# Optimization experiments

Measured on AMD Instinct MI355X. Metric: run time of the kernel, lower is better.

The kernel has to match this reference:

```python
import jax, jax.numpy as jnp
import numpy as np

B, S, D, H = 2, 2048, 1024, 16
HD = D // H  # 64
MASK_VAL = -10000.0


def setup_inputs() -> dict:
    key = jax.random.key(0)
    ks = jax.random.split(key, 8)
    sc = 0.02
    q_features = jax.random.normal(ks[0], (B, S, D), jnp.float32)
    kv_features = jax.random.normal(ks[1], (B, S, D), jnp.float32)
    # causal mask, broadcastable (1,1,S,S)
    mask = jnp.tril(jnp.ones((S, S), jnp.bool_))[None, None]
    Wq = jax.random.normal(ks[2], (D, D), jnp.float32) * sc
    bq = jnp.zeros((D,), jnp.float32)
    Wkv = jax.random.normal(ks[3], (D, 2 * D), jnp.float32) * sc
    bkv = jnp.zeros((2 * D,), jnp.float32)
    Wp = jax.random.normal(ks[4], (D, D), jnp.float32) * sc
    bp = jnp.zeros((D,), jnp.float32)
    return {"q_features": q_features, "kv_features": kv_features, "mask": mask,
            "Wq": Wq, "bq": bq, "Wkv": Wkv, "bkv": bkv, "Wp": Wp, "bp": bp}


def _split_heads(t):
    # (B,S,D) -> (B,H,S,HD)
    return t.reshape(B, S, H, HD).transpose(0, 2, 1, 3)


def reference(q_features, kv_features, mask, Wq, bq, Wkv, bkv, Wp, bp):
    query = q_features @ Wq + bq            # (B,S,D)
    kv = kv_features @ Wkv + bkv            # (B,S,2D)
    key, value = jnp.split(kv, 2, axis=-1)
    q = _split_heads(query)                 # (B,H,S,HD)
    k = _split_heads(key)
    v = _split_heads(value)
    scores = jnp.einsum('bhqd,bhkd->bhqk', q, k) / jnp.sqrt(jnp.float32(HD))
    scores = jnp.where(mask, scores, jnp.asarray(MASK_VAL, scores.dtype))
    attn = jax.nn.softmax(scores, axis=-1)  # (B,H,S,S)
    out = jnp.einsum('bhqk,bhkd->bhqd', attn, v)
    out = out.transpose(0, 2, 1, 3).reshape(B, S, D)  # merge heads
    return out @ Wp + bp
```

## Files before the change

### kernel.cpp

```cpp
#include <hip/hip_runtime.h>

typedef unsigned short u16;
typedef unsigned int u32;
typedef __attribute__((ext_vector_type(4))) unsigned short us4;
typedef __attribute__((ext_vector_type(8))) unsigned short us8;
typedef __attribute__((ext_vector_type(4))) short s16x4;
typedef __attribute__((ext_vector_type(8))) __bf16 bf16x8;
typedef __attribute__((ext_vector_type(4))) float floatx4;

#define S_ 2048
#define D_ 1024
#define QSC 0.18033688f

__device__ __forceinline__ float b2f(u16 u) {
  unsigned v = ((unsigned)u) << 16;
  return __builtin_bit_cast(float, v);
}
__device__ __forceinline__ u16 f2bf(float f) {
  unsigned u = __builtin_bit_cast(unsigned, f);
  unsigned r = (u + 0x7fffu + ((u >> 16) & 1u)) >> 16;
  return (u16)r;
}
__device__ __forceinline__ u16 f2bf_rhu(float f) {
  return (u16)((__builtin_bit_cast(unsigned, f) + 0x8000u) >> 16);
}

typedef const __attribute__((address_space(1))) u32* gas_t;
typedef __attribute__((address_space(3))) u32* las_t;
__device__ __forceinline__ void gload16(const u16* g, u16* l) {
  __builtin_amdgcn_global_load_lds((gas_t)g, (las_t)l, 16, 0, 0);
}

__global__ __launch_bounds__(256) void prep(
    const float* __restrict__ qf, const float* __restrict__ kvf,
    const float* __restrict__ Wq, const float* __restrict__ Wkv,
    const float* __restrict__ Wp, u16* __restrict__ qa, u16* __restrict__ kva,
    u16* __restrict__ Wqt, u16* __restrict__ Wkvt, u16* __restrict__ Wpt) {
  int bid = blockIdx.x, tid = threadIdx.x;
  if (bid < 4096) {
    const float* src = (bid < 2048) ? qf : kvf;
    u16* dst = (bid < 2048) ? qa : kva;
    size_t i = ((size_t)(bid & 2047) * 256 + tid) * 8;
    floatx4 a = *(const floatx4*)(src + i);
    floatx4 b = *(const floatx4*)(src + i + 4);
    us8 r;
#pragma unroll
    for (int j = 0; j < 4; j++) { r[j] = f2bf(a[j]); r[4 + j] = f2bf(b[j]); }
    *(us8*)(dst + i) = r;
  } else {
    int t = bid - 4096;
    const float* src; u16* dst; int R, C;
    if (t < 1024)      { src = Wq;  dst = Wqt;  R = 1024; C = 1024; }
    else if (t < 3072) { t -= 1024; src = Wkv; dst = Wkvt; R = 1024; C = 2048; }
    else               { t -= 3072; src = Wp;  dst = Wpt;  R = 1024; C = 1024; }
    int bx = t % (C >> 5), by = t / (C >> 5);
    __shared__ u16 tile[32][33];
    int tx = tid & 31, ty = tid >> 5;
    int x = bx * 32 + tx;
    for (int i = ty; i < 32; i += 8)
      tile[i][tx] = f2bf(src[(size_t)(by * 32 + i) * C + x]);
    __syncthreads();
    int ox = by * 32 + tx;
    for (int i = ty; i < 32; i += 8)
      dst[(size_t)(bx * 32 + i) * R + ox] = tile[tx][i];
  }
}

template <int TM, int TN, int MODE>
__device__ __forceinline__ void gemm_core(
    const u16* __restrict__ A, const u16* __restrict__ Bt,
    const float* __restrict__ bias, void* __restrict__ C0,
    u16* __restrict__ C1, int N, int n0, int m0,
    u16* As, u16* Bs, float cscale) {
  constexpr int MT = TM / 32, NT = TN / 32;
  int tid  = threadIdx.x;
  int wave = tid >> 6, lane = tid & 63;
  int quad = lane >> 4, l16 = lane & 15;
  int wr = wave >> 1, wc = wave & 1;
  const u16* Ag = A  + (size_t)(m0 + wave * 8 + (lane >> 3)) * 1024 + (lane & 7) * 8;
  const u16* Bg = Bt + (size_t)(n0 + wave * 8 + (lane >> 3)) * 1024 + (lane & 7) * 8;
  u16* Aw = As + wave * 8 * 64;
  u16* Bw = Bs + wave * 8 * 64;
  floatx4 acc[MT][NT] = {};
  for (int k0 = 0; k0 < 1024; k0 += 64) {
    if (k0) __syncthreads();
#pragma unroll
    for (int p = 0; p < TM / 32; p++)
      gload16(Ag + (size_t)p * 32 * 1024 + k0, Aw + p * 32 * 64);
#pragma unroll
    for (int p = 0; p < TN / 32; p++)
      gload16(Bg + (size_t)p * 32 * 1024 + k0, Bw + p * 32 * 64);
    __syncthreads();
#pragma unroll
    for (int kk = 0; kk < 2; kk++) {
      bf16x8 af[MT], bf[NT];
#pragma unroll
      for (int mt = 0; mt < MT; mt++)
        af[mt] = __builtin_bit_cast(bf16x8,
            *(const us8*)&As[(wr * (TM / 2) + mt * 16 + l16) * 64 + (kk * 4 + quad) * 8]);
#pragma unroll
      for (int nt = 0; nt < NT; nt++)
        bf[nt] = __builtin_bit_cast(bf16x8,
            *(const us8*)&Bs[(wc * (TN / 2) + nt * 16 + l16) * 64 + (kk * 4 + quad) * 8]);
#pragma unroll
      for (int mt = 0; mt < MT; mt++)
#pragma unroll
        for (int nt = 0; nt < NT; nt++)
          acc[mt][nt] = __builtin_amdgcn_mfma_f32_16x16x32_bf16(
              af[mt], bf[nt], acc[mt][nt], 0, 0, 0);
    }
  }
#pragma unroll
  for (int mt = 0; mt < MT; mt++) {
#pragma unroll
    for (int nt = 0; nt < NT; nt++) {
      int col  = n0 + wc * (TN / 2) + nt * 16 + l16;
      int rowq = m0 + wr * (TM / 2) + mt * 16 + quad * 4;
      float bv = bias[col];
      if (MODE == 0) {
        u16* o = (u16*)C0;
#pragma unroll
        for (int r = 0; r < 4; r++)
          o[(size_t)(rowq + r) * N + col] = f2bf((acc[mt][nt][r] + bv) * cscale);
      } else if (MODE == 1) {
        float* o = (float*)C0;
#pragma unroll
        for (int r = 0; r < 4; r++)
          o[(size_t)(rowq + r) * N + col] = acc[mt][nt][r] + bv;
      } else {
        if (col < 1024) {
          u16* o = (u16*)C0;
#pragma unroll
          for (int r = 0; r < 4; r++)
            o[(size_t)(rowq + r) * 1024 + col] = f2bf(acc[mt][nt][r] + bv);
        } else {
          int vcol = col - 1024;
          int b = rowq >> 11, s0 = rowq & 2047;
          us4 pv;
#pragma unroll
          for (int r = 0; r < 4; r++) pv[r] = f2bf(acc[mt][nt][r] + bv);
          *(us4*)&C1[((size_t)(b * 1024 + vcol)) * (size_t)S_ + s0] = pv;
        }
      }
    }
  }
}

__global__ __launch_bounds__(256) void gemm_qkv(
    const u16* __restrict__ qa, const u16* __restrict__ kva,
    const u16* __restrict__ Wqt, const u16* __restrict__ Wkvt,
    const float* __restrict__ bq, const float* __restrict__ bkv,
    u16* __restrict__ Qb, u16* __restrict__ Kb, u16* __restrict__ Vt) {
  __shared__ __align__(16) u16 As[128 * 64];
  __shared__ __align__(16) u16 Bs[128 * 64];
  int bid = blockIdx.x;
  if (bid < 256) {
    gemm_core<128, 128, 0>(qa, Wqt, bq, Qb, nullptr, 1024,
                           (bid & 7) * 128, (bid >> 3) * 128, As, Bs, QSC);
  } else {
    int lb = bid - 256;
    gemm_core<128, 128, 2>(kva, Wkvt, bkv, Kb, Vt, 2048,
                           (lb & 15) * 128, (lb >> 4) * 128, As, Bs, 1.0f);
  }
}

__global__ __launch_bounds__(256) void gemm_out(
    const u16* __restrict__ AO, const u16* __restrict__ Wpt,
    const float* __restrict__ bp, float* __restrict__ out) {
  __shared__ __align__(16) u16 As[64 * 64];
  __shared__ __align__(16) u16 Bs[128 * 64];
  gemm_core<64, 128, 1>(AO, Wpt, bp, out, nullptr, 1024,
                        (blockIdx.x & 7) * 128, (blockIdx.x >> 3) * 64, As, Bs, 1.0f);
}

__global__ __launch_bounds__(256) void attn_fwd(
    const u16* __restrict__ Q, const u16* __restrict__ Kb,
    const u16* __restrict__ Vt, u16* __restrict__ O,
    u16* __restrict__ Opart, float* __restrict__ ml) {
  __shared__ __align__(16) u16 Ks[64 * 64];
  __shared__ __align__(16) u16 Vs[64 * 64];
  int tid  = threadIdx.x;
  int wave = tid >> 6, lane = tid & 63;
  int quad = lane >> 4, l16 = lane & 15;
  int bh = blockIdx.x, b = bh >> 4, h = bh & 15;
  int y = blockIdx.y;
  int qt, kb0, kb1, half = 0;
  bool split = (y < 32);
  if (split) {
    qt = 31 - (y >> 1);
    half = y & 1;
    int h1 = (qt + 1) >> 1;
    kb0 = half ? h1 : 0;
    kb1 = half ? (qt + 1) : h1;
  } else {
    qt = 47 - y;
    kb0 = 0; kb1 = qt + 1;
  }
  const size_t row0 = (size_t)b * S_;
  const u16* Kg = Kb + row0 * D_ + h * 64;
  const u16* Vg = Vt + ((size_t)b * 1024 + h * 64) * S_;

  int qrow = qt * 64 + wave * 16 + l16;
  const u16* qp = Q + (row0 + qrow) * D_ + h * 64 + quad * 8;
  bf16x8 aqv[2];
  aqv[0] = __builtin_bit_cast(bf16x8, *(const us8*)(qp));
  aqv[1] = __builtin_bit_cast(bf16x8, *(const us8*)(qp + 32));

  floatx4 o_[4] = {};
  floatx4 l_acc = {};
  const s16x4 ones4 = {0x3F80, 0x3F80, 0x3F80, 0x3F80};

  int lr = lane >> 3, c8 = lane & 7;
  int r0 = wave * 16 + lr;
  int r1 = r0 + 8;
  us8 pk0 = *(const us8*)(Kg + (size_t)(kb0 * 64 + r0) * D_ + c8 * 8);
  us8 pk1 = *(const us8*)(Kg + (size_t)(kb0 * 64 + r1) * D_ + c8 * 8);
  us8 pv0 = *(const us8*)(Vg + (size_t)r0 * S_ + kb0 * 64 + c8 * 8);
  us8 pv1 = *(const us8*)(Vg + (size_t)r1 * S_ + kb0 * 64 + c8 * 8);

  for (int kb = kb0; kb < kb1; kb++) {
    __syncthreads();
    *(us8*)&Ks[r0 * 64 + ((c8 ^ (r0 & 7)) << 3)] = pk0;
    *(us8*)&Ks[r1 * 64 + ((c8 ^ (r1 & 7)) << 3)] = pk1;
    *(us8*)&Vs[r0 * 64 + ((c8 ^ (r0 & 7)) << 3)] = pv0;
    *(us8*)&Vs[r1 * 64 + ((c8 ^ (r1 & 7)) << 3)] = pv1;
    if (kb + 1 < kb1) {
      int koff = (kb + 1) * 64;
      pk0 = *(const us8*)(Kg + (size_t)(koff + r0) * D_ + c8 * 8);
      pk1 = *(const us8*)(Kg + (size_t)(koff + r1) * D_ + c8 * 8);
      pv0 = *(const us8*)(Vg + (size_t)r0 * S_ + koff + c8 * 8);
      pv1 = *(const us8*)(Vg + (size_t)r1 * S_ + koff + c8 * 8);
    }
    __syncthreads();

    floatx4 s[4] = {};
#pragma unroll
    for (int kk = 0; kk < 2; kk++)
#pragma unroll
      for (int nt = 0; nt < 4; nt++) {
        us8 kf = *(const us8*)&Ks[(nt * 16 + l16) * 64 +
                                  (((kk * 4 + quad) ^ (l16 & 7)) << 3)];
        s[nt] = __builtin_amdgcn_mfma_f32_16x16x32_bf16(
            __builtin_bit_cast(bf16x8, kf), aqv[kk], s[nt], 0, 0, 0);
      }

    if (kb == qt) {
      int qg = wave * 16 + l16;
#pragma unroll
      for (int nt = 0; nt < 4; nt++)
#pragma unroll
        for (int r = 0; r < 4; r++)
          if (nt * 16 + quad * 4 + r > qg) s[nt][r] = -1e5f;
    }

    s16x4 pb[4];
#pragma unroll
    for (int nt = 0; nt < 4; nt++)
#pragma unroll
      for (int r = 0; r < 4; r++)
        pb[nt][r] = (short)f2bf_rhu(__builtin_amdgcn_exp2f(s[nt][r]));

#pragma unroll
    for (int nt = 0; nt < 4; nt++) {
      l_acc = __builtin_amdgcn_mfma_f32_16x16x16bf16_1k(ones4, pb[nt], l_acc, 0, 0, 0);
#pragma unroll
      for (int mt = 0; mt < 4; mt++) {
        int hd = mt * 16 + l16;
        int chunk = nt * 2 + (quad >> 1);
        us4 vf = *(const us4*)&Vs[hd * 64 + ((chunk ^ (l16 & 7)) << 3) + (quad & 1) * 4];
        o_[mt] = __builtin_amdgcn_mfma_f32_16x16x16bf16_1k(
            __builtin_bit_cast(s16x4, vf), pb[nt], o_[mt], 0, 0, 0);
      }
    }
  }

  if (!split) {
    float rl = __builtin_amdgcn_rcpf(l_acc[0]);
    size_t orow = (row0 + qt * 64 + wave * 16 + l16) * D_ + h * 64;
#pragma unroll
    for (int mt = 0; mt < 4; mt++) {
      us4 ov;
#pragma unroll
      for (int r = 0; r < 4; r++) ov[r] = f2bf(o_[mt][r] * rl);
      *(us4*)&O[orow + mt * 16 + quad * 4] = ov;
    }
  } else {
    int pb_ = (qt - 16) * 2 + half;
    u16* op = Opart + ((size_t)(bh * 32 + pb_)) * 4096;
    int qrow_l = wave * 16 + l16;
#pragma unroll
    for (int mt = 0; mt < 4; mt++) {
      us4 ov;
#pragma unroll
      for (int r = 0; r < 4; r++) ov[r] = f2bf(o_[mt][r]);
      *(us4*)&op[qrow_l * 64 + mt * 16 + quad * 4] = ov;
    }
    if (quad == 0)
      ml[(size_t)(bh * 32 + pb_) * 64 + qrow_l] = l_acc[0];
  }
}

__global__ __launch_bounds__(256) void combine(
    const u16* __restrict__ Opart, const float* __restrict__ ml,
    u16* __restrict__ O) {
  int bh = blockIdx.x, b = bh >> 4, h = bh & 15;
  int qt = 16 + blockIdx.y;
  int base = bh * 32 + (qt - 16) * 2;
  const u16* o1 = Opart + (size_t)base * 4096;
  const u16* o2 = o1 + 4096;
  int row = threadIdx.x >> 2, cg = (threadIdx.x & 3) * 16;
  float l1 = ml[(size_t)base * 64 + row];
  float l2 = ml[(size_t)(base + 1) * 64 + row];
  float inv = __builtin_amdgcn_rcpf(l1 + l2);
  size_t orow = ((size_t)b * S_ + qt * 64 + row) * D_ + h * 64 + cg;
#pragma unroll
  for (int v = 0; v < 2; v++) {
    us8 x1 = *(const us8*)&o1[row * 64 + cg + v * 8];
    us8 x2 = *(const us8*)&o2[row * 64 + cg + v * 8];
    us8 out;
#pragma unroll
    for (int j = 0; j < 8; j++)
      out[j] = f2bf((b2f(x1[j]) + b2f(x2[j])) * inv);
    *(us8*)&O[orow + v * 8] = out;
  }
}

extern "C" void kernel_launch(void* const* d_in, const int* in_sizes, int n_in,
                              void* d_out, int out_size, void* d_ws, size_t ws_size,
                              hipStream_t stream) {
  const float* qf  = (const float*)d_in[0];
  const float* kvf = (const float*)d_in[1];
  const float* Wq  = (const float*)d_in[3];
  const float* bq  = (const float*)d_in[4];
  const float* Wkv = (const float*)d_in[5];
  const float* bkv = (const float*)d_in[6];
  const float* Wp  = (const float*)d_in[7];
  const float* bp  = (const float*)d_in[8];

  char* ws = (char*)d_ws;
  const size_t MB = 1048576;
  u16*   kva  = (u16*)(ws);
  u16*   AO   = (u16*)(ws);
  u16*   Kbp  = (u16*)(ws + 8 * MB);
  u16*   Vtp  = (u16*)(ws + 16 * MB);
  u16*   Wqt  = (u16*)(ws + 24 * MB);
  float* mlp  = (float*)(ws + 24 * MB);
  u16*   Wkvt = (u16*)(ws + 26 * MB);
  u16*   Wpt  = (u16*)(ws + 30 * MB);
  u16*   qa    = (u16*)d_out;
  u16*   Opart = (u16*)d_out;
  u16*   Qb    = (u16*)d_out + (size_t)4 * 1048576;

  prep<<<8192, 256, 0, stream>>>(qf, kvf, Wq, Wkv, Wp, qa, kva, Wqt, Wkvt, Wpt);
  gemm_qkv<<<768, 256, 0, stream>>>(qa, kva, Wqt, Wkvt, bq, bkv, Qb, Kbp, Vtp);
  attn_fwd<<<dim3(32, 48), 256, 0, stream>>>(Qb, Kbp, Vtp, AO, Opart, mlp);
  combine<<<dim3(32, 16), 256, 0, stream>>>(Opart, mlp, AO);
  gemm_out<<<512, 256, 0, stream>>>(AO, Wpt, bp, (float*)d_out);
}
```

Baseline: 229.0 us.

## Rewrite QKV GEMM as 256x256 tile with 4-stage async LDS pipeline

Replaces the 128x128 QKV projection GEMM with a 512-thread kernel computing 256x256 tiles. It uses a 4-stage ring of direct global-to-LDS loads with XOR-swizzled layout, split A/B phases with barriers, and raised priority around MFMA bursts. The aim is to raise data reuse per tile and hide global-load latency behind MFMA work. The cost is a 128KB LDS footprint and only 192 blocks, which can leave CUs underused and weakens occupancy.

Result: faster. 217.4 us (-5.0%).

```diff
diff --git a/kernel.cpp b/kernel.cpp
--- a/kernel.cpp
+++ b/kernel.cpp
@@ -30,6 +30,16 @@
 __device__ __forceinline__ void gload16(const u16* g, u16* l) {
   __builtin_amdgcn_global_load_lds((gas_t)g, (las_t)l, 16, 0, 0);
 }
+
+#define PBAR()                                   \
+  {                                              \
+    __builtin_amdgcn_sched_barrier(0);           \
+    asm volatile("" ::: "memory");               \
+    __builtin_amdgcn_s_barrier();                \
+    asm volatile("" ::: "memory");               \
+    __builtin_amdgcn_sched_barrier(0);           \
+  }
+#define WAITVM(N) asm volatile("s_waitcnt vmcnt(" #N ")" ::: "memory")
 
 __global__ __launch_bounds__(256) void prep(
     const float* __restrict__ qf, const float* __restrict__ kvf,
@@ -66,6 +76,148 @@
   }
 }
 
+template <int MODE>
+__device__ __forceinline__ void gemm256(
+    const u16* __restrict__ A, const u16* __restrict__ Bt,
+    const float* __restrict__ bias, void* __restrict__ C0,
+    u16* __restrict__ C1, int N, int m0, int n0, u16* smem, float cscale) {
+  int tid = threadIdx.x;
+  int w = tid >> 6, lane = tid & 63;
+  int quad = lane >> 4, l16 = lane & 15;
+  int wr = w >> 2, wc = w & 3;
+
+  int srow = w * 32 + (lane >> 2);
+  int gchunk = ((lane & 3) ^ ((lane >> 3) & 3)) << 3;
+  const u16* Asrc = A + (size_t)(m0 + srow) * 1024 + gchunk;
+  const u16* Bsrc = Bt + (size_t)(n0 + srow) * 1024 + gchunk;
+  u16* Adst = smem + w * 1024;
+  u16* Bdst = smem + 32768 + w * 1024;
+
+  int swz = (quad ^ ((l16 >> 1) & 3)) << 3;
+  int aoff = (wr * 128 + l16) * 32 + swz;
+  int boff = 32768 + (wc * 64 + l16) * 32 + swz;
+
+  floatx4 acc[8][4] = {};
+
+#define STAGE_A(t)                                             \
+  {                                                            \
+    int s_ = (t) & 3;                                          \
+    gload16(Asrc + (t) * 32, Adst + s_ * 8192);                \
+    gload16(Asrc + (t) * 32 + 16384, Adst + s_ * 8192 + 512);  \
+  }
+#define STAGE_B(t)                                             \
+  {                                                            \
+    int s_ = (t) & 3;                                          \
+    gload16(Bsrc + (t) * 32, Bdst + s_ * 8192);                \
+    gload16(Bsrc + (t) * 32 + 16384, Bdst + s_ * 8192 + 512);  \
+  }
+
+  STAGE_A(0); STAGE_B(0); STAGE_A(1); STAGE_B(1); STAGE_A(2); STAGE_B(2);
+  WAITVM(8);
+  PBAR();
+
+  bf16x8 af[4], bf[4];
+
+#define PHASE_A(t, DOSTAGE)                                                 \
+  {                                                                         \
+    int s_ = (t) & 3;                                                       \
+    _Pragma("unroll") for (int mf = 0; mf < 4; mf++)                        \
+        af[mf] = __builtin_bit_cast(                                        \
+            bf16x8, *(const us8*)&smem[s_ * 8192 + aoff + mf * 512]);       \
+    _Pragma("unroll") for (int nf = 0; nf < 4; nf++)                        \
+        bf[nf] = __builtin_bit_cast(                                        \
+            bf16x8, *(const us8*)&smem[s_ * 8192 + boff + nf * 512]);       \
+    if (DOSTAGE) STAGE_A((t) + 3);                                          \
+    PBAR();                                                                 \
+    __builtin_amdgcn_s_setprio(1);                                          \
+    _Pragma("unroll") for (int mf = 0; mf < 4; mf++)                        \
+        _Pragma("unroll") for (int nf = 0; nf < 4; nf++)                    \
+            acc[mf][nf] = __builtin_amdgcn_mfma_f32_16x16x32_bf16(          \
+                af[mf], bf[nf], acc[mf][nf], 0, 0, 0);                      \
+    __builtin_amdgcn_s_setprio(0);                                          \
+    PBAR();                                                                 \
+  }
+#define PHASE_B(t, DOSTAGE, VMW)                                            \
+  {                                                                         \
+    int s_ = (t) & 3;                                                       \
+    _Pragma("unroll") for (int mf = 0; mf < 4; mf++)                        \
+        af[mf] = __builtin_bit_cast(                                        \
+            bf16x8,                                                         \
+            *(const us8*)&smem[s_ * 8192 + aoff + 2048 + mf * 512]);        \
+    if (DOSTAGE) STAGE_B((t) + 3);                                          \
+    PBAR();                                                                 \
+    __builtin_amdgcn_s_setprio(1);                                          \
+    _Pragma("unroll") for (int mf = 0; mf < 4; mf++)                        \
+        _Pragma("unroll") for (int nf = 0; nf < 4; nf++)                    \
+            acc[4 + mf][nf] = __builtin_amdgcn_mfma_f32_16x16x32_bf16(      \
+                af[mf], bf[nf], acc[4 + mf][nf], 0, 0, 0);                  \
+    __builtin_amdgcn_s_setprio(0);                                          \
+    VMW;                                                                    \
+    PBAR();                                                                 \
+  }
+
+#pragma unroll 1
+  for (int t = 0; t < 29; t++) {
+    PHASE_A(t, true);
+    PHASE_B(t, true, WAITVM(4));
+  }
+  PHASE_A(29, false); PHASE_B(29, false, (void)0);
+  PHASE_A(30, false); PHASE_B(30, false, WAITVM(0));
+  PHASE_A(31, false); PHASE_B(31, false, (void)0);
+
+#undef PHASE_A
+#undef PHASE_B
+#undef STAGE_A
+#undef STAGE_B
+
+#pragma unroll
+  for (int mf = 0; mf < 8; mf++) {
+#pragma unroll
+    for (int nf = 0; nf < 4; nf++) {
+      int col = n0 + wc * 64 + nf * 16 + l16;
+      int rowq = m0 + wr * 128 + mf * 16 + quad * 4;
+      float bv = bias[col];
+      if (MODE == 0) {
+        u16* o = (u16*)C0;
+#pragma unroll
+        for (int r = 0; r < 4; r++)
+          o[(size_t)(rowq + r) * N + col] = f2bf((acc[mf][nf][r] + bv) * cscale);
+      } else {
+        if (col < 1024) {
+          u16* o = (u16*)C0;
+#pragma unroll
+          for (int r = 0; r < 4; r++)
+            o[(size_t)(rowq + r) * 1024 + col] = f2bf(acc[mf][nf][r] + bv);
+        } else {
+          int vcol = col - 1024;
+          int b = rowq >> 11, s0 = rowq & 2047;
+          us4 pv;
+#pragma unroll
+          for (int r = 0; r < 4; r++) pv[r] = f2bf(acc[mf][nf][r] + bv);
+          *(us4*)&C1[((size_t)(b * 1024 + vcol)) * (size_t)S_ + s0] = pv;
+        }
+      }
+    }
+  }
+}
+
+__global__ __launch_bounds__(512, 2) void gemm_qkv(
+    const u16* __restrict__ qa, const u16* __restrict__ kva,
+    const u16* __restrict__ Wqt, const u16* __restrict__ Wkvt,
+    const float* __restrict__ bq, const float* __restrict__ bkv,
+    u16* __restrict__ Qb, u16* __restrict__ Kb, u16* __restrict__ Vt) {
+  __shared__ __align__(16) u16 smem[65536];
+  int bid = blockIdx.x;
+  if (bid < 64) {
+    gemm256<0>(qa, Wqt, bq, Qb, nullptr, 1024,
+               (bid >> 2) * 256, (bid & 3) * 256, smem, QSC);
+  } else {
+    int lb = bid - 64;
+    gemm256<2>(kva, Wkvt, bkv, Kb, Vt, 2048,
+               (lb >> 3) * 256, (lb & 7) * 256, smem, 1.0f);
+  }
+}
+
 template <int TM, int TN, int MODE>
 __device__ __forceinline__ void gemm_core(
     const u16* __restrict__ A, const u16* __restrict__ Bt,
@@ -143,24 +295,6 @@
         }
       }
     }
-  }
-}
-
-__global__ __launch_bounds__(256) void gemm_qkv(
-    const u16* __restrict__ qa, const u16* __restrict__ kva,
-    const u16* __restrict__ Wqt, const u16* __restrict__ Wkvt,
-    const float* __restrict__ bq, const float* __restrict__ bkv,
-    u16* __restrict__ Qb, u16* __restrict__ Kb, u16* __restrict__ Vt) {
-  __shared__ __align__(16) u16 As[128 * 64];
-  __shared__ __align__(16) u16 Bs[128 * 64];
-  int bid = blockIdx.x;
-  if (bid < 256) {
-    gemm_core<128, 128, 0>(qa, Wqt, bq, Qb, nullptr, 1024,
-                           (bid & 7) * 128, (bid >> 3) * 128, As, Bs, QSC);
-  } else {
-    int lb = bid - 256;
-    gemm_core<128, 128, 2>(kva, Wkvt, bkv, Kb, Vt, 2048,
-                           (lb & 15) * 128, (lb >> 4) * 128, As, Bs, 1.0f);
   }
 }
 
@@ -352,7 +486,7 @@
   u16*   Qb    = (u16*)d_out + (size_t)4 * 1048576;
 
   prep<<<8192, 256, 0, stream>>>(qf, kvf, Wq, Wkv, Wp, qa, kva, Wqt, Wkvt, Wpt);
-  gemm_qkv<<<768, 256, 0, stream>>>(qa, kva, Wqt, Wkvt, bq, bkv, Qb, Kbp, Vtp);
+  gemm_qkv<<<192, 512, 0, stream>>>(qa, kva, Wqt, Wkvt, bq, bkv, Qb, Kbp, Vtp);
   attn_fwd<<<dim3(32, 48), 256, 0, stream>>>(Qb, Kbp, Vtp, AO, Opart, mlp);
   combine<<<dim3(32, 16), 256, 0, stream>>>(Opart, mlp, AO);
   gemm_out<<<512, 256, 0, stream>>>(AO, Wpt, bp, (float*)d_out);
```
